# Performance work log

Measured on AMD Instinct MI355X. Metric: run time of the kernel, lower is better.

The kernel has to match this reference:

```python
import jax, jax.numpy as jnp
import numpy as np

# SuperposedExpert: K parallel TT-factorized FFN paths + holographic routing.
# d_model=1024 factorized as [32,32]; d_ff=4096 as [64,64]; tt_ranks=[1,16,1] (r0/r2 squeezed).
K, D_MODEL, D_FF, RANK = 4, 1024, 4096, 16
IN1, IN2 = 32, 32          # factorize_for_tt(d_model)
F1, F2 = 64, 64            # factorize_for_tt(d_ff)
TEMP = 1.0                 # routing_temperature


def setup_inputs() -> dict:
    key = jax.random.key(0)
    ks = jax.random.split(key, 8)
    s = 0.05
    tokens = jax.random.normal(ks[0], (2048, D_MODEL), dtype=jnp.float32)
    # TT cores for ffn1: d_model -> d_ff  (input_dims [32,32], output_dims [64,64])
    ffn1_core1 = jax.random.normal(ks[1], (K, IN1, F1, RANK), dtype=jnp.float32) * s
    ffn1_core2 = jax.random.normal(ks[2], (K, RANK, IN2, F2), dtype=jnp.float32) * s
    # TT cores for ffn2: d_ff -> d_model (input_dims [64,64], output_dims [32,32])
    ffn2_core1 = jax.random.normal(ks[3], (K, F1, IN1, RANK), dtype=jnp.float32) * s
    ffn2_core2 = jax.random.normal(ks[4], (K, RANK, F2, IN2), dtype=jnp.float32) * s
    # Holographic routing params (hd_dim == d_model -> identity HD projection)
    pb = jax.random.normal(ks[5], (K, D_MODEL), dtype=jnp.float32)
    path_bases = pb / jnp.linalg.norm(pb, axis=-1, keepdims=True)  # orthogonal-ish init
    path_weights = jax.random.normal(ks[6], (K, D_MODEL), dtype=jnp.float32) * s
    return {
        'tokens': tokens,
        'ffn1_core1': ffn1_core1, 'ffn1_core2': ffn1_core2,
        'ffn2_core1': ffn2_core1, 'ffn2_core2': ffn2_core2,
        'path_bases': path_bases, 'path_weights': path_weights,
    }


def reference(tokens, ffn1_core1, ffn1_core2, ffn2_core1, ffn2_core2,
              path_bases, path_weights):
    N = tokens.shape[0]
    # ---- K superposed TT-FFN paths ----
    x3 = tokens.reshape(N, IN1, IN2)  # [n, a, b]
    # TT matmul 1: y[x,y] = sum_{a,b,r} G1[a,x,r] G2[r,b,y] x[a,b]
    h = jnp.einsum('nab,kaxr,krby->knxy', x3, ffn1_core1, ffn1_core2)
    h = jax.nn.gelu(h.reshape(K, N, D_FF))  # quantum_activation stand-in
    h3 = h.reshape(K, N, F1, F2)
    y = jnp.einsum('knab,kaxr,krby->knxy', h3, ffn2_core1, ffn2_core2)
    y = y.reshape(K, N, D_MODEL)  # per-path outputs
    # ---- Holographic HD routing (hd_dim == d_model: identity projection) ----
    logits = jnp.einsum('nd,kd->nk', tokens, path_bases) / TEMP
    gates = jax.nn.softmax(logits, axis=-1)  # [n, k]
    # Collapse superposition: per-path elementwise HD modulation + gated sum
    out = jnp.einsum('knd,kd,nk->nd', y, 1.0 + path_weights, gates)
    return out
```

## Files before the change

### kernel.cpp

```cpp
#include <hip/hip_runtime.h>
#include <stdint.h>

#define GAS __attribute__((address_space(1)))
#define LAS __attribute__((address_space(3)))

typedef __attribute__((ext_vector_type(8))) short short8;
typedef __attribute__((ext_vector_type(16))) float f32x16;
typedef __attribute__((ext_vector_type(4))) float f32x4;

static constexpr int N_TOK = 2048;
static constexpr int DM    = 1024;
static constexpr int DF    = 4096;
static constexpr int KP    = 4;

__device__ inline unsigned short f2bf(float f) {
  union { float f; uint32_t u; } v; v.f = f;
  uint32_t u = v.u;
  u += 0x7FFFu + ((u >> 16) & 1u);
  return (unsigned short)(u >> 16);
}

__device__ inline uint32_t pk_bf(float lo, float hi) {
  union { float f; uint32_t u; } a, b; a.f = lo; b.f = hi;
  uint32_t ul = a.u + 0x7FFFu + ((a.u >> 16) & 1u);
  uint32_t uh = b.u + 0x7FFFu + ((b.u >> 16) & 1u);
  return (ul >> 16) | (uh & 0xFFFF0000u);
}

__device__ inline float gelu_gate(float v, float g) {
  float t0 = v * v;
  float u  = v * __builtin_fmaf(t0, -0.10294456f, -2.3022539f);
  float e  = __builtin_amdgcn_exp2f(u);
  float r  = __builtin_amdgcn_rcpf(1.0f + e);
  return v * g * r;
}

__device__ inline void gld16(const void* g, void* l) {
  __builtin_amdgcn_global_load_lds((const GAS void*)g, (LAS void*)l, 16, 0, 0);
}

__global__ __launch_bounds__(256) void setup_kernel(
    const float* __restrict__ tokens, const float* __restrict__ pb,
    const float* __restrict__ c11, const float* __restrict__ c12,
    const float* __restrict__ c21, const float* __restrict__ c22,
    float* __restrict__ gates, unsigned short* __restrict__ xb,
    unsigned short* __restrict__ w1t, unsigned short* __restrict__ w2t) {
  __shared__ __align__(16) float sh[17472];
  const int blk = blockIdx.x;
  const int t = threadIdx.x;
  if (blk < 1024) {
    const int k = blk >> 8, x = (blk >> 2) & 63, y0 = (blk & 3) * 16;
    float* s1  = sh;
    float* s2T = sh + 512;
    if (t < 128) {
      int a = t >> 2, rq = (t & 3) * 4;
      *(float4*)(s1 + a * 16 + rq) =
          *(const float4*)(c11 + (((size_t)(k * 32 + a)) * 64 + x) * 16 + rq);
    }
#pragma unroll
    for (int j = 0; j < 8; ++j) {
      int i = t + j * 256;
      int rb = i >> 2, yy0 = (i & 3) * 4;
      float4 v = *(const float4*)(c12 + (size_t)(k * 16) * 2048 + (size_t)rb * 64 + y0 + yy0);
      s2T[(yy0 + 0) * 524 + rb] = v.x;
      s2T[(yy0 + 1) * 524 + rb] = v.y;
      s2T[(yy0 + 2) * 524 + rb] = v.z;
      s2T[(yy0 + 3) * 524 + rb] = v.w;
    }
    __syncthreads();
    const int a = t >> 3, b0 = (t & 7) * 4;
    float4 s1q[4];
#pragma unroll
    for (int q = 0; q < 4; ++q) s1q[q] = *(const float4*)(s1 + a * 16 + q * 4);
    const float* a0s = (const float*)s1q;
    for (int y = 0; y < 16; ++y) {
      const float* s2y = s2T + y * 524;
      float4 acc = {0.f, 0.f, 0.f, 0.f};
#pragma unroll
      for (int r = 0; r < 16; ++r) {
        float cv = a0s[r];
        float4 bv = *(const float4*)(s2y + r * 32 + b0);
        acc.x = __builtin_fmaf(cv, bv.x, acc.x);
        acc.y = __builtin_fmaf(cv, bv.y, acc.y);
        acc.z = __builtin_fmaf(cv, bv.z, acc.z);
        acc.w = __builtin_fmaf(cv, bv.w, acc.w);
      }
      ushort4 o; o.x = f2bf(acc.x); o.y = f2bf(acc.y); o.z = f2bf(acc.z); o.w = f2bf(acc.w);
      *(ushort4*)(w1t + ((size_t)k * DF + x * 64 + y0 + y) * DM + t * 4) = o;
    }
  } else if (blk < 1280) {
    const int bb = blk - 1024;
    const int k = bb >> 6, x = (bb >> 1) & 31, y0 = (bb & 1) * 16;
    float* s1  = sh;
    float* s2T = sh + 1024;
    {
      int a = t >> 2, rq = (t & 3) * 4;
      *(float4*)(s1 + a * 16 + rq) =
          *(const float4*)(c21 + (((size_t)(k * 64 + a)) * 32 + x) * 16 + rq);
    }
#pragma unroll
    for (int j = 0; j < 16; ++j) {
      int i = t + j * 256;
      int rb = i >> 2, yy0 = (i & 3) * 4;
      float4 v = *(const float4*)(c22 + (size_t)(k * 16) * 2048 + (size_t)rb * 32 + y0 + yy0);
      s2T[(yy0 + 0) * 1028 + rb] = v.x;
      s2T[(yy0 + 1) * 1028 + rb] = v.y;
      s2T[(yy0 + 2) * 1028 + rb] = v.z;
      s2T[(yy0 + 3) * 1028 + rb] = v.w;
    }
    __syncthreads();
    const int b0 = (t & 15) * 4;
#pragma unroll
    for (int jj = 0; jj < 4; ++jj) {
      const int a = (t >> 4) + jj * 16;
      float4 s1q[4];
#pragma unroll
      for (int q = 0; q < 4; ++q) s1q[q] = *(const float4*)(s1 + a * 16 + q * 4);
      const float* a0s = (const float*)s1q;
      for (int y = 0; y < 16; ++y) {
        const float* s2y = s2T + y * 1028;
        float4 acc = {0.f, 0.f, 0.f, 0.f};
#pragma unroll
        for (int r = 0; r < 16; ++r) {
          float cv = a0s[r];
          float4 bv = *(const float4*)(s2y + r * 64 + b0);
          acc.x = __builtin_fmaf(cv, bv.x, acc.x);
          acc.y = __builtin_fmaf(cv, bv.y, acc.y);
          acc.z = __builtin_fmaf(cv, bv.z, acc.z);
          acc.w = __builtin_fmaf(cv, bv.w, acc.w);
        }
        ushort4 o; o.x = f2bf(acc.x); o.y = f2bf(acc.y); o.z = f2bf(acc.z); o.w = f2bf(acc.w);
        *(ushort4*)(w2t + ((size_t)k * DM + x * 32 + y0 + y) * DF + t * 4 + jj * 1024) = o;
      }
    }
  } else {
    const int wave = t >> 6, lane = t & 63;
    const int n = (blk - 1280) * 4 + wave;
    float s0 = 0.f, s1v = 0.f, s2v = 0.f, s3v = 0.f;
    const float4* tr = (const float4*)(tokens + (size_t)n * DM);
#pragma unroll
    for (int j = 0; j < 4; ++j) {
      int idx = j * 64 + lane;
      float4 tv = tr[idx];
      ushort4 b;
      b.x = f2bf(tv.x); b.y = f2bf(tv.y); b.z = f2bf(tv.z); b.w = f2bf(tv.w);
      *(ushort4*)(xb + (size_t)n * DM + idx * 4) = b;
      float4 q;
      q = ((const float4*)(pb + 0 * DM))[idx]; s0  += tv.x*q.x + tv.y*q.y + tv.z*q.z + tv.w*q.w;
      q = ((const float4*)(pb + 1 * DM))[idx]; s1v += tv.x*q.x + tv.y*q.y + tv.z*q.z + tv.w*q.w;
      q = ((const float4*)(pb + 2 * DM))[idx]; s2v += tv.x*q.x + tv.y*q.y + tv.z*q.z + tv.w*q.w;
      q = ((const float4*)(pb + 3 * DM))[idx]; s3v += tv.x*q.x + tv.y*q.y + tv.z*q.z + tv.w*q.w;
    }
#pragma unroll
    for (int off = 32; off > 0; off >>= 1) {
      s0  += __shfl_xor(s0, off);
      s1v += __shfl_xor(s1v, off);
      s2v += __shfl_xor(s2v, off);
      s3v += __shfl_xor(s3v, off);
    }
    if (lane == 0) {
      float m = fmaxf(fmaxf(s0, s1v), fmaxf(s2v, s3v));
      float e0 = __expf(s0 - m), e1 = __expf(s1v - m), e2 = __expf(s2v - m), e3 = __expf(s3v - m);
      float inv = 1.0f / (e0 + e1 + e2 + e3);
      float4 g; g.x = e0 * inv; g.y = e1 * inv; g.z = e2 * inv; g.w = e3 * inv;
      *(float4*)(gates + n * 4) = g;
    }
  }
}

#define PH_SYNC(V) do { \
    asm volatile("s_waitcnt vmcnt(" #V ")" ::: "memory"); \
    __builtin_amdgcn_s_barrier(); \
    __builtin_amdgcn_sched_barrier(0); \
  } while (0)

#define G1_TILE(KT, BO, WO, V0, V1, V2) do { \
    const int kn_ = ((KT) + 1) * 64; \
    const bool st_ = (KT) < 15; \
     \
    PH_SYNC(V0); \
    if (st_) { const unsigned short* s_ = Wg + (size_t)srow * DM + kn_ + lch * 8; \
      gld16(s_, smem + (WO) + t * 16); gld16(s_ + 64 * DM, smem + (WO) + 8192 + t * 16); } \
    _Pragma("unroll") for (int fi = 0; fi < 4; ++fi) \
      _Pragma("unroll") for (int s = 0; s < 2; ++s) \
        af[fi][s] = *(const short8*)(smem + (BO) + aRowB + fi * 2048 + (cxor16 ^ (s * 64) ^ (fi * 32))); \
    _Pragma("unroll") for (int ti = 0; ti < 2; ++ti) \
      _Pragma("unroll") for (int s = 0; s < 2; ++s) \
        bf0[ti][s] = *(const short8*)(smem + (BO) + xRowB + ti * 2048 + (cxor16 ^ (s * 64) ^ wnx64 ^ (ti * 32))); \
    __builtin_amdgcn_s_setprio(1); \
    _Pragma("unroll") for (int fi = 0; fi < 4; ++fi) \
      _Pragma("unroll") for (int ti = 0; ti < 2; ++ti) { \
        acc[0][0][fi][ti] = __builtin_amdgcn_mfma_f32_16x16x32_bf16(af[fi][0], bf0[ti][0], acc[0][0][fi][ti], 0, 0, 0); \
        acc[0][0][fi][ti] = __builtin_amdgcn_mfma_f32_16x16x32_bf16(af[fi][1], bf0[ti][1], acc[0][0][fi][ti], 0, 0, 0); } \
    __builtin_amdgcn_s_setprio(0); \
     \
    PH_SYNC(V1); \
    if (st_) { const unsigned short* s_ = Xg + (size_t)srow * DM + kn_ + lch * 8; \
      gld16(s_, smem + (WO) + 32768 + t * 16); gld16(s_ + 64 * DM, smem + (WO) + 32768 + 8192 + t * 16); } \
    _Pragma("unroll") for (int ti = 0; ti < 2; ++ti) \
      _Pragma("unroll") for (int s = 0; s < 2; ++s) \
        bf1[ti][s] = *(const short8*)(smem + (BO) + xRowB + 16384 + ti * 2048 + (cxor16 ^ (s * 64) ^ wnx64 ^ (ti * 32))); \
    __builtin_amdgcn_s_setprio(1); \
    _Pragma("unroll") for (int fi = 0; fi < 4; ++fi) \
      _Pragma("unroll") for (int ti = 0; ti < 2; ++ti) { \
        acc[0][1][fi][ti] = __builtin_amdgcn_mfma_f32_16x16x32_bf16(af[fi][0], bf1[ti][0], acc[0][1][fi][ti], 0, 0, 0); \
        acc[0][1][fi][ti] = __builtin_amdgcn_mfma_f32_16x16x32_bf16(af[fi][1], bf1[ti][1], acc[0][1][fi][ti], 0, 0, 0); } \
    __builtin_amdgcn_s_setprio(0); \
     \
    PH_SYNC(V2); \
    if (st_) { const unsigned short* s_ = Xg + (size_t)(128 + srow) * DM + kn_ + lch * 8; \
      gld16(s_, smem + (WO) + 32768 + 16384 + t * 16); gld16(s_ + 64 * DM, smem + (WO) + 32768 + 16384 + 8192 + t * 16); } \
    _Pragma("unroll") for (int fi = 0; fi < 4; ++fi) \
      _Pragma("unroll") for (int s = 0; s < 2; ++s) \
        af[fi][s] = *(const short8*)(smem + (BO) + aRowB + 16384 + fi * 2048 + (cxor16 ^ (s * 64) ^ (fi * 32))); \
    __builtin_amdgcn_s_setprio(1); \
    _Pragma("unroll") for (int fi = 0; fi < 4; ++fi) \
      _Pragma("unroll") for (int ti = 0; ti < 2; ++ti) { \
        acc[1][1][fi][ti] = __builtin_amdgcn_mfma_f32_16x16x32_bf16(af[fi][0], bf1[ti][0], acc[1][1][fi][ti], 0, 0, 0); \
        acc[1][1][fi][ti] = __builtin_amdgcn_mfma_f32_16x16x32_bf16(af[fi][1], bf1[ti][1], acc[1][1][fi][ti], 0, 0, 0); } \
    __builtin_amdgcn_s_setprio(0); \
     \
    if (st_) { const unsigned short* s_ = Wg + (size_t)(128 + srow) * DM + kn_ + lch * 8; \
      gld16(s_, smem + (WO) + 16384 + t * 16); gld16(s_ + 64 * DM, smem + (WO) + 16384 + 8192 + t * 16); } \
    __builtin_amdgcn_s_setprio(1); \
    _Pragma("unroll") for (int fi = 0; fi < 4; ++fi) \
      _Pragma("unroll") for (int ti = 0; ti < 2; ++ti) { \
        acc[1][0][fi][ti] = __builtin_amdgcn_mfma_f32_16x16x32_bf16(af[fi][0], bf0[ti][0], acc[1][0][fi][ti], 0, 0, 0); \
        acc[1][0][fi][ti] = __builtin_amdgcn_mfma_f32_16x16x32_bf16(af[fi][1], bf0[ti][1], acc[1][0][fi][ti], 0, 0, 0); } \
    __builtin_amdgcn_s_setprio(0); \
  } while (0)

__global__ __launch_bounds__(512, 1) void gemm1(
    const unsigned short* __restrict__ xb, const unsigned short* __restrict__ w1t,
    const float* __restrict__ gates, unsigned short* __restrict__ hg) {
  __shared__ __align__(16) char smem[131072];
  const int t = threadIdx.x, lane = t & 63, wv = t >> 6;
  const int wm = wv >> 2, wn = wv & 3;
  const int hw = blockIdx.x + (blockIdx.y << 3) + (blockIdx.z << 7);
  const int lg = (hw & 7) * 64 + (hw >> 3);
  const int m0 = (lg & 7) * 256;
  const int f0 = ((lg >> 3) & 15) * 256;
  const int kp = lg >> 7;
  const unsigned short* __restrict__ Wg = w1t + (size_t)kp * DF * DM + (size_t)f0 * DM;
  const unsigned short* __restrict__ Xg = xb + (size_t)m0 * DM;

  const int srow = t >> 3;
  const int lch  = (t & 7) ^ (srow & 7) ^ (srow >> 3);
  const int l15 = lane & 15, kg = lane >> 4;
  const int cxor16 = (kg ^ (lane & 7) ^ (l15 >> 3)) * 16;
  const int wnx64  = (wn & 1) * 64;
  const int aRowB  = (wm * 64 + l15) * 128;
  const int xRowB  = 32768 + (wn * 32 + l15) * 128;

  f32x4 acc[2][2][4][2] = {};
  short8 af[4][2], bf0[2][2], bf1[2][2];

  {
    const unsigned short* sw = Wg + (size_t)srow * DM + lch * 8;
    const unsigned short* sx = Xg + (size_t)srow * DM + lch * 8;
    gld16(sw,            smem + t * 16);
    gld16(sw + 64 * DM,  smem + 8192 + t * 16);
    gld16(sx,            smem + 32768 + t * 16);
    gld16(sx + 64 * DM,  smem + 32768 + 8192 + t * 16);
    gld16(sx + 128 * DM, smem + 32768 + 16384 + t * 16);
    gld16(sx + 192 * DM, smem + 32768 + 16384 + 8192 + t * 16);
    gld16(sw + 128 * DM, smem + 16384 + t * 16);
    gld16(sw + 192 * DM, smem + 16384 + 8192 + t * 16);
  }

#pragma unroll 1
  for (int kt = 0; kt < 14; kt += 2) {
    G1_TILE(kt,     0,     65536, 4, 4, 4);
    G1_TILE(kt + 1, 65536, 0,     4, 4, 4);
  }
  G1_TILE(14, 0,     65536, 4, 4, 4);
  G1_TILE(15, 65536, 0,     4, 2, 0);

  unsigned short* __restrict__ H = hg + (size_t)kp * N_TOK * DF;
#pragma unroll
  for (int cB = 0; cB < 2; ++cB)
#pragma unroll
    for (int ti = 0; ti < 2; ++ti) {
      const int tok = m0 + cB * 128 + wn * 32 + ti * 16 + l15;
      const float g = gates[tok * 4 + kp];
      unsigned short* hrow = H + (size_t)tok * DF + f0 + wm * 64 + kg * 4;
#pragma unroll
      for (int rA = 0; rA < 2; ++rA)
#pragma unroll
        for (int fi = 0; fi < 4; ++fi) {
          f32x4 v = acc[rA][cB][fi][ti];
          float r0 = gelu_gate(v.x, g);
          float r1 = gelu_gate(v.y, g);
          float r2 = gelu_gate(v.z, g);
          float r3 = gelu_gate(v.w, g);
          uint2 p; p.x = pk_bf(r0, r1); p.y = pk_bf(r2, r3);
          *(uint2*)(hrow + rA * 128 + fi * 16) = p;
        }
    }
}

#define G2_TILE(KT, BO, WO, V0, V1, V2) do { \
    const int kn_ = ((KT) + 1) * 64; \
    const bool st_ = (KT) < 63; \
     \
    PH_SYNC(V0); \
    if (st_) gld16(Wg + (size_t)srow * DF + kn_ + lch * 8, smem + (WO) + t * 16); \
    _Pragma("unroll") for (int fi = 0; fi < 2; ++fi) \
      _Pragma("unroll") for (int s = 0; s < 2; ++s) \
        af[fi][s] = *(const short8*)(smem + (BO) + awRowB + fi * 2048 + (cxor16 ^ awx ^ (fi * 32) ^ (s * 64))); \
    _Pragma("unroll") for (int ti = 0; ti < 2; ++ti) \
      _Pragma("unroll") for (int s = 0; s < 2; ++s) \
        bf0[ti][s] = *(const short8*)(smem + (BO) + xRowB + ti * 2048 + (cxor16 ^ wnx64 ^ (ti * 32) ^ (s * 64))); \
    __builtin_amdgcn_s_setprio(1); \
    _Pragma("unroll") for (int fi = 0; fi < 2; ++fi) \
      _Pragma("unroll") for (int ti = 0; ti < 2; ++ti) { \
        acc[0][0][fi][ti] = __builtin_amdgcn_mfma_f32_16x16x32_bf16(af[fi][0], bf0[ti][0], acc[0][0][fi][ti], 0, 0, 0); \
        acc[0][0][fi][ti] = __builtin_amdgcn_mfma_f32_16x16x32_bf16(af[fi][1], bf0[ti][1], acc[0][0][fi][ti], 0, 0, 0); } \
    __builtin_amdgcn_s_setprio(0); \
     \
    PH_SYNC(V1); \
    if (st_) { const unsigned short* s_ = Xg + (size_t)srow * DF + kn_ + lch * 8; \
      gld16(s_, smem + (WO) + 16384 + t * 16); gld16(s_ + 64 * DF, smem + (WO) + 16384 + 8192 + t * 16); } \
    _Pragma("unroll") for (int ti = 0; ti < 2; ++ti) \
      _Pragma("unroll") for (int s = 0; s < 2; ++s) \
        bf1[ti][s] = *(const short8*)(smem + (BO) + xRowB + 16384 + ti * 2048 + (cxor16 ^ wnx64 ^ (ti * 32) ^ (s * 64))); \
    __builtin_amdgcn_s_setprio(1); \
    _Pragma("unroll") for (int fi = 0; fi < 2; ++fi) \
      _Pragma("unroll") for (int ti = 0; ti < 2; ++ti) { \
        acc[0][1][fi][ti] = __builtin_amdgcn_mfma_f32_16x16x32_bf16(af[fi][0], bf1[ti][0], acc[0][1][fi][ti], 0, 0, 0); \
        acc[0][1][fi][ti] = __builtin_amdgcn_mfma_f32_16x16x32_bf16(af[fi][1], bf1[ti][1], acc[0][1][fi][ti], 0, 0, 0); } \
    __builtin_amdgcn_s_setprio(0); \
     \
    PH_SYNC(V2); \
    if (st_) { const unsigned short* s_ = Xg + (size_t)(128 + srow) * DF + kn_ + lch * 8; \
      gld16(s_, smem + (WO) + 32768 + t * 16); gld16(s_ + 64 * DF, smem + (WO) + 32768 + 8192 + t * 16); } \
    _Pragma("unroll") for (int fi = 0; fi < 2; ++fi) \
      _Pragma("unroll") for (int s = 0; s < 2; ++s) \
        af[fi][s] = *(const short8*)(smem + (BO) + awRowB + 8192 + fi * 2048 + (cxor16 ^ awx ^ (fi * 32) ^ (s * 64))); \
    __builtin_amdgcn_s_setprio(1); \
    _Pragma("unroll") for (int fi = 0; fi < 2; ++fi) \
      _Pragma("unroll") for (int ti = 0; ti < 2; ++ti) { \
        acc[1][1][fi][ti] = __builtin_amdgcn_mfma_f32_16x16x32_bf16(af[fi][0], bf1[ti][0], acc[1][1][fi][ti], 0, 0, 0); \
        acc[1][1][fi][ti] = __builtin_amdgcn_mfma_f32_16x16x32_bf16(af[fi][1], bf1[ti][1], acc[1][1][fi][ti], 0, 0, 0); } \
    __builtin_amdgcn_s_setprio(0); \
     \
    if (st_) gld16(Wg + (size_t)(64 + srow) * DF + kn_ + lch * 8, smem + (WO) + 8192 + t * 16); \
    __builtin_amdgcn_s_setprio(1); \
    _Pragma("unroll") for (int fi = 0; fi < 2; ++fi) \
      _Pragma("unroll") for (int ti = 0; ti < 2; ++ti) { \
        acc[1][0][fi][ti] = __builtin_amdgcn_mfma_f32_16x16x32_bf16(af[fi][0], bf0[ti][0], acc[1][0][fi][ti], 0, 0, 0); \
        acc[1][0][fi][ti] = __builtin_amdgcn_mfma_f32_16x16x32_bf16(af[fi][1], bf0[ti][1], acc[1][0][fi][ti], 0, 0, 0); } \
    __builtin_amdgcn_s_setprio(0); \
  } while (0)

__global__ __launch_bounds__(512, 1) void gemm2(
    const unsigned short* __restrict__ hg, const unsigned short* __restrict__ w2t,
    const float* __restrict__ pw, float* __restrict__ part) {
  __shared__ __align__(16) char smem[98304];
  const int t = threadIdx.x, lane = t & 63, wv = t >> 6;
  const int wm = wv >> 2, wn = wv & 3;
  const int hw = blockIdx.x + (blockIdx.y << 3) + (blockIdx.z << 6);
  const int lg = (hw & 7) * 32 + (hw >> 3);
  const int m0 = (lg & 7) * 256;
  const int n0 = ((lg >> 3) & 7) * 128;
  const int kp = lg >> 6;
  const unsigned short* __restrict__ Wg = w2t + (size_t)kp * DM * DF + (size_t)n0 * DF;
  const unsigned short* __restrict__ Xg = hg + (size_t)kp * N_TOK * DF + (size_t)m0 * DF;

  const int srow = t >> 3;
  const int lch  = (t & 7) ^ (srow & 7) ^ (srow >> 3);
  const int l15 = lane & 15, kg = lane >> 4;
  const int cxor16 = (kg ^ (lane & 7) ^ (l15 >> 3)) * 16;
  const int wnx64  = (wn & 1) * 64;
  const int awx    = wm * 64;
  const int awRowB = (wm * 32 + l15) * 128;
  const int xRowB  = 16384 + (wn * 32 + l15) * 128;

  f32x4 acc[2][2][2][2] = {};
  short8 af[2][2], bf0[2][2], bf1[2][2];

  {
    const unsigned short* sw = Wg + (size_t)srow * DF + lch * 8;
    const unsigned short* sx = Xg + (size_t)srow * DF + lch * 8;
    gld16(sw,            smem + t * 16);
    gld16(sx,            smem + 16384 + t * 16);
    gld16(sx + 64 * DF,  smem + 16384 + 8192 + t * 16);
    gld16(sx + 128 * DF, smem + 32768 + t * 16);
    gld16(sx + 192 * DF, smem + 32768 + 8192 + t * 16);
    gld16(sw + 64 * DF,  smem + 8192 + t * 16);
  }

#pragma unroll 1
  for (int kt = 0; kt < 62; kt += 2) {
    G2_TILE(kt,     0,     49152, 3, 2, 3);
    G2_TILE(kt + 1, 49152, 0,     3, 2, 3);
  }
  G2_TILE(62, 0,     49152, 3, 2, 3);
  G2_TILE(63, 49152, 0,     3, 1, 0);

  float* __restrict__ P = part + (size_t)kp * N_TOK * DM;
  float4 pwv[2][2];
#pragma unroll
  for (int rA = 0; rA < 2; ++rA)
#pragma unroll
    for (int fi = 0; fi < 2; ++fi) {
      float4 w = *(const float4*)(pw + kp * DM + n0 + rA * 64 + wm * 32 + fi * 16 + kg * 4);
      pwv[rA][fi].x = 1.0f + w.x; pwv[rA][fi].y = 1.0f + w.y;
      pwv[rA][fi].z = 1.0f + w.z; pwv[rA][fi].w = 1.0f + w.w;
    }
#pragma unroll
  for (int cB = 0; cB < 2; ++cB)
#pragma unroll
    for (int ti = 0; ti < 2; ++ti) {
      const int tok = m0 + cB * 128 + wn * 32 + ti * 16 + l15;
      float* prow = P + (size_t)tok * DM + n0 + wm * 32 + kg * 4;
#pragma unroll
      for (int rA = 0; rA < 2; ++rA)
#pragma unroll
        for (int fi = 0; fi < 2; ++fi) {
          f32x4 v = acc[rA][cB][fi][ti];
          float4 o;
          o.x = pwv[rA][fi].x * v.x;
          o.y = pwv[rA][fi].y * v.y;
          o.z = pwv[rA][fi].z * v.z;
          o.w = pwv[rA][fi].w * v.w;
          *(float4*)(prow + rA * 64 + fi * 16) = o;
        }
    }
}

__global__ __launch_bounds__(256) void reduce_k(
    const float* __restrict__ part, float* __restrict__ out) {
  const size_t i = ((size_t)blockIdx.x * 256 + threadIdx.x) * 4;
  const size_t S = (size_t)N_TOK * DM;
  float4 a = *(const float4*)(part + i);
  float4 b = *(const float4*)(part + S + i);
  float4 c = *(const float4*)(part + 2 * S + i);
  float4 d = *(const float4*)(part + 3 * S + i);
  float4 r;
  r.x = a.x + b.x + c.x + d.x;
  r.y = a.y + b.y + c.y + d.y;
  r.z = a.z + b.z + c.z + d.z;
  r.w = a.w + b.w + c.w + d.w;
  *(float4*)(out + i) = r;
}

extern "C" void kernel_launch(void* const* d_in, const int* in_sizes, int n_in,
                              void* d_out, int out_size, void* d_ws, size_t ws_size,
                              hipStream_t stream) {
  const float* tokens = (const float*)d_in[0];
  const float* f1c1   = (const float*)d_in[1];
  const float* f1c2   = (const float*)d_in[2];
  const float* f2c1   = (const float*)d_in[3];
  const float* f2c2   = (const float*)d_in[4];
  const float* pb     = (const float*)d_in[5];
  const float* pw     = (const float*)d_in[6];
  float* out = (float*)d_out;

  char* ws = (char*)d_ws;
  unsigned short* xb  = (unsigned short*)(ws);
  unsigned short* w1t = (unsigned short*)(ws + (4ull  << 20));
  float*          part = (float*)(ws + (4ull << 20));
  unsigned short* w2t = (unsigned short*)(ws + (36ull << 20));
  unsigned short* hg  = (unsigned short*)(ws + (68ull << 20));
  float*          gates = (float*)(ws + (132ull << 20));

  hipLaunchKernelGGL(setup_kernel, dim3(1792), dim3(256), 0, stream,
                     tokens, pb, f1c1, f1c2, f2c1, f2c2, gates, xb, w1t, w2t);
  hipLaunchKernelGGL(gemm1, dim3(8, 16, KP), dim3(512), 0, stream, xb, w1t, gates, hg);
  hipLaunchKernelGGL(gemm2, dim3(8, 8, KP), dim3(512), 0, stream, hg, w2t, pw, part);
  hipLaunchKernelGGL(reduce_k, dim3(2048), dim3(256), 0, stream, part, out);
}
```

Measured before the change: 243.9 us.

## Prefetch next tile's A/B fragments into registers across phases in both GEMMs

Restructures the per-tile phase schedule of both GEMM kernels so that the first A and B fragments of the next K-tile are loaded from LDS during the last phase of the current tile. Separate lo/hi A-fragment registers and ping-ponged B0 buffers are added, and the vmcnt wait points are reordered. The goal is to hide LDS read latency behind MFMA work and cut stalls at the start of each tile. In exchange, register pressure goes up at one block per CU, and the reworked wait counts must still cover every outstanding global-to-LDS load.

```diff
diff --git a/kernel.cpp b/kernel.cpp
--- a/kernel.cpp
+++ b/kernel.cpp
@@ -168,67 +168,68 @@
   }
 }
 
-#define PH_SYNC(V) do { \
-    asm volatile("s_waitcnt vmcnt(" #V ")" ::: "memory"); \
-    __builtin_amdgcn_s_barrier(); \
-    __builtin_amdgcn_sched_barrier(0); \
-  } while (0)
-
-#define G1_TILE(KT, BO, WO, V0, V1, V2) do { \
-    const int kn_ = ((KT) + 1) * 64; \
-    const bool st_ = (KT) < 15; \
-     \
-    PH_SYNC(V0); \
-    if (st_) { const unsigned short* s_ = Wg + (size_t)srow * DM + kn_ + lch * 8; \
-      gld16(s_, smem + (WO) + t * 16); gld16(s_ + 64 * DM, smem + (WO) + 8192 + t * 16); } \
+#define VMC(N) asm volatile("s_waitcnt vmcnt(" #N ")" ::: "memory")
+#define BARS do { __builtin_amdgcn_s_barrier(); __builtin_amdgcn_sched_barrier(0); } while (0)
+
+#define G1T(KT, BO, WO, B0C, B0N, V0S, V1S, PREF3) do { \
+  const int kn_ = ((KT) + 1) * 64; \
+  const bool st_ = (KT) < 15; \
+   \
+  VMC(V0S); BARS; \
+  _Pragma("unroll") for (int ti = 0; ti < 2; ++ti) \
+    _Pragma("unroll") for (int s = 0; s < 2; ++s) \
+      bf1[ti][s] = *(const short8*)(smem + (BO) + xRowB + 16384 + ti * 2048 + (cxor16 ^ (s * 64) ^ wnx64 ^ (ti * 32))); \
+  if (st_) { const unsigned short* s_ = Wg + (size_t)srow * DM + kn_ + lch * 8; \
+    gld16(s_, smem + (WO) + t * 16); gld16(s_ + 64 * DM, smem + (WO) + 8192 + t * 16); } \
+  __builtin_amdgcn_s_setprio(1); \
+  _Pragma("unroll") for (int fi = 0; fi < 4; ++fi) \
+    _Pragma("unroll") for (int ti = 0; ti < 2; ++ti) { \
+      acc[0][0][fi][ti] = __builtin_amdgcn_mfma_f32_16x16x32_bf16(af_lo[fi][0], B0C[ti][0], acc[0][0][fi][ti], 0, 0, 0); \
+      acc[0][0][fi][ti] = __builtin_amdgcn_mfma_f32_16x16x32_bf16(af_lo[fi][1], B0C[ti][1], acc[0][0][fi][ti], 0, 0, 0); } \
+  __builtin_amdgcn_s_setprio(0); \
+   \
+  VMC(V1S); BARS; \
+  _Pragma("unroll") for (int fi = 0; fi < 4; ++fi) \
+    _Pragma("unroll") for (int s = 0; s < 2; ++s) \
+      af_hi[fi][s] = *(const short8*)(smem + (BO) + aRowB + 16384 + fi * 2048 + (cxor16 ^ (s * 64) ^ (fi * 32))); \
+  if (st_) { const unsigned short* s_ = Xg + (size_t)srow * DM + kn_ + lch * 8; \
+    gld16(s_, smem + (WO) + 32768 + t * 16); gld16(s_ + 64 * DM, smem + (WO) + 32768 + 8192 + t * 16); } \
+  __builtin_amdgcn_s_setprio(1); \
+  _Pragma("unroll") for (int fi = 0; fi < 4; ++fi) \
+    _Pragma("unroll") for (int ti = 0; ti < 2; ++ti) { \
+      acc[0][1][fi][ti] = __builtin_amdgcn_mfma_f32_16x16x32_bf16(af_lo[fi][0], bf1[ti][0], acc[0][1][fi][ti], 0, 0, 0); \
+      acc[0][1][fi][ti] = __builtin_amdgcn_mfma_f32_16x16x32_bf16(af_lo[fi][1], bf1[ti][1], acc[0][1][fi][ti], 0, 0, 0); } \
+  __builtin_amdgcn_s_setprio(0); \
+   \
+  BARS; \
+  if (st_) { const unsigned short* s_ = Xg + (size_t)(128 + srow) * DM + kn_ + lch * 8; \
+    gld16(s_, smem + (WO) + 32768 + 16384 + t * 16); gld16(s_ + 64 * DM, smem + (WO) + 32768 + 16384 + 8192 + t * 16); } \
+  __builtin_amdgcn_s_setprio(1); \
+  _Pragma("unroll") for (int fi = 0; fi < 4; ++fi) \
+    _Pragma("unroll") for (int ti = 0; ti < 2; ++ti) { \
+      acc[1][1][fi][ti] = __builtin_amdgcn_mfma_f32_16x16x32_bf16(af_hi[fi][0], bf1[ti][0], acc[1][1][fi][ti], 0, 0, 0); \
+      acc[1][1][fi][ti] = __builtin_amdgcn_mfma_f32_16x16x32_bf16(af_hi[fi][1], bf1[ti][1], acc[1][1][fi][ti], 0, 0, 0); } \
+  __builtin_amdgcn_s_setprio(0); \
+   \
+  if (PREF3) { VMC(2); } \
+  BARS; \
+  if (PREF3) { \
     _Pragma("unroll") for (int fi = 0; fi < 4; ++fi) \
       _Pragma("unroll") for (int s = 0; s < 2; ++s) \
-        af[fi][s] = *(const short8*)(smem + (BO) + aRowB + fi * 2048 + (cxor16 ^ (s * 64) ^ (fi * 32))); \
+        af_lo[fi][s] = *(const short8*)(smem + (WO) + aRowB + fi * 2048 + (cxor16 ^ (s * 64) ^ (fi * 32))); \
     _Pragma("unroll") for (int ti = 0; ti < 2; ++ti) \
       _Pragma("unroll") for (int s = 0; s < 2; ++s) \
-        bf0[ti][s] = *(const short8*)(smem + (BO) + xRowB + ti * 2048 + (cxor16 ^ (s * 64) ^ wnx64 ^ (ti * 32))); \
-    __builtin_amdgcn_s_setprio(1); \
-    _Pragma("unroll") for (int fi = 0; fi < 4; ++fi) \
-      _Pragma("unroll") for (int ti = 0; ti < 2; ++ti) { \
-        acc[0][0][fi][ti] = __builtin_amdgcn_mfma_f32_16x16x32_bf16(af[fi][0], bf0[ti][0], acc[0][0][fi][ti], 0, 0, 0); \
-        acc[0][0][fi][ti] = __builtin_amdgcn_mfma_f32_16x16x32_bf16(af[fi][1], bf0[ti][1], acc[0][0][fi][ti], 0, 0, 0); } \
-    __builtin_amdgcn_s_setprio(0); \
-     \
-    PH_SYNC(V1); \
-    if (st_) { const unsigned short* s_ = Xg + (size_t)srow * DM + kn_ + lch * 8; \
-      gld16(s_, smem + (WO) + 32768 + t * 16); gld16(s_ + 64 * DM, smem + (WO) + 32768 + 8192 + t * 16); } \
-    _Pragma("unroll") for (int ti = 0; ti < 2; ++ti) \
-      _Pragma("unroll") for (int s = 0; s < 2; ++s) \
-        bf1[ti][s] = *(const short8*)(smem + (BO) + xRowB + 16384 + ti * 2048 + (cxor16 ^ (s * 64) ^ wnx64 ^ (ti * 32))); \
-    __builtin_amdgcn_s_setprio(1); \
-    _Pragma("unroll") for (int fi = 0; fi < 4; ++fi) \
-      _Pragma("unroll") for (int ti = 0; ti < 2; ++ti) { \
-        acc[0][1][fi][ti] = __builtin_amdgcn_mfma_f32_16x16x32_bf16(af[fi][0], bf1[ti][0], acc[0][1][fi][ti], 0, 0, 0); \
-        acc[0][1][fi][ti] = __builtin_amdgcn_mfma_f32_16x16x32_bf16(af[fi][1], bf1[ti][1], acc[0][1][fi][ti], 0, 0, 0); } \
-    __builtin_amdgcn_s_setprio(0); \
-     \
-    PH_SYNC(V2); \
-    if (st_) { const unsigned short* s_ = Xg + (size_t)(128 + srow) * DM + kn_ + lch * 8; \
-      gld16(s_, smem + (WO) + 32768 + 16384 + t * 16); gld16(s_ + 64 * DM, smem + (WO) + 32768 + 16384 + 8192 + t * 16); } \
-    _Pragma("unroll") for (int fi = 0; fi < 4; ++fi) \
-      _Pragma("unroll") for (int s = 0; s < 2; ++s) \
-        af[fi][s] = *(const short8*)(smem + (BO) + aRowB + 16384 + fi * 2048 + (cxor16 ^ (s * 64) ^ (fi * 32))); \
-    __builtin_amdgcn_s_setprio(1); \
-    _Pragma("unroll") for (int fi = 0; fi < 4; ++fi) \
-      _Pragma("unroll") for (int ti = 0; ti < 2; ++ti) { \
-        acc[1][1][fi][ti] = __builtin_amdgcn_mfma_f32_16x16x32_bf16(af[fi][0], bf1[ti][0], acc[1][1][fi][ti], 0, 0, 0); \
-        acc[1][1][fi][ti] = __builtin_amdgcn_mfma_f32_16x16x32_bf16(af[fi][1], bf1[ti][1], acc[1][1][fi][ti], 0, 0, 0); } \
-    __builtin_amdgcn_s_setprio(0); \
-     \
-    if (st_) { const unsigned short* s_ = Wg + (size_t)(128 + srow) * DM + kn_ + lch * 8; \
-      gld16(s_, smem + (WO) + 16384 + t * 16); gld16(s_ + 64 * DM, smem + (WO) + 16384 + 8192 + t * 16); } \
-    __builtin_amdgcn_s_setprio(1); \
-    _Pragma("unroll") for (int fi = 0; fi < 4; ++fi) \
-      _Pragma("unroll") for (int ti = 0; ti < 2; ++ti) { \
-        acc[1][0][fi][ti] = __builtin_amdgcn_mfma_f32_16x16x32_bf16(af[fi][0], bf0[ti][0], acc[1][0][fi][ti], 0, 0, 0); \
-        acc[1][0][fi][ti] = __builtin_amdgcn_mfma_f32_16x16x32_bf16(af[fi][1], bf0[ti][1], acc[1][0][fi][ti], 0, 0, 0); } \
-    __builtin_amdgcn_s_setprio(0); \
-  } while (0)
+        B0N[ti][s] = *(const short8*)(smem + (WO) + xRowB + ti * 2048 + (cxor16 ^ (s * 64) ^ wnx64 ^ (ti * 32))); \
+  } \
+  if (st_) { const unsigned short* s_ = Wg + (size_t)(128 + srow) * DM + kn_ + lch * 8; \
+    gld16(s_, smem + (WO) + 16384 + t * 16); gld16(s_ + 64 * DM, smem + (WO) + 16384 + 8192 + t * 16); } \
+  __builtin_amdgcn_s_setprio(1); \
+  _Pragma("unroll") for (int fi = 0; fi < 4; ++fi) \
+    _Pragma("unroll") for (int ti = 0; ti < 2; ++ti) { \
+      acc[1][0][fi][ti] = __builtin_amdgcn_mfma_f32_16x16x32_bf16(af_hi[fi][0], B0C[ti][0], acc[1][0][fi][ti], 0, 0, 0); \
+      acc[1][0][fi][ti] = __builtin_amdgcn_mfma_f32_16x16x32_bf16(af_hi[fi][1], B0C[ti][1], acc[1][0][fi][ti], 0, 0, 0); } \
+  __builtin_amdgcn_s_setprio(0); \
+} while (0)
 
 __global__ __launch_bounds__(512, 1) void gemm1(
     const unsigned short* __restrict__ xb, const unsigned short* __restrict__ w1t,
@@ -253,7 +254,7 @@
   const int xRowB  = 32768 + (wn * 32 + l15) * 128;
 
   f32x4 acc[2][2][4][2] = {};
-  short8 af[4][2], bf0[2][2], bf1[2][2];
+  short8 af_lo[4][2], af_hi[4][2], bf0p[2][2], bf0q[2][2], bf1[2][2];
 
   {
     const unsigned short* sw = Wg + (size_t)srow * DM + lch * 8;
@@ -267,14 +268,25 @@
     gld16(sw + 128 * DM, smem + 16384 + t * 16);
     gld16(sw + 192 * DM, smem + 16384 + 8192 + t * 16);
   }
+  VMC(4); BARS;
+#pragma unroll
+  for (int fi = 0; fi < 4; ++fi)
+#pragma unroll
+    for (int s = 0; s < 2; ++s)
+      af_lo[fi][s] = *(const short8*)(smem + aRowB + fi * 2048 + (cxor16 ^ (s * 64) ^ (fi * 32)));
+#pragma unroll
+  for (int ti = 0; ti < 2; ++ti)
+#pragma unroll
+    for (int s = 0; s < 2; ++s)
+      bf0p[ti][s] = *(const short8*)(smem + xRowB + ti * 2048 + (cxor16 ^ (s * 64) ^ wnx64 ^ (ti * 32)));
 
 #pragma unroll 1
   for (int kt = 0; kt < 14; kt += 2) {
-    G1_TILE(kt,     0,     65536, 4, 4, 4);
-    G1_TILE(kt + 1, 65536, 0,     4, 4, 4);
+    G1T(kt,     0,     65536, bf0p, bf0q, 2, 2, 1);
+    G1T(kt + 1, 65536, 0,     bf0q, bf0p, 2, 2, 1);
   }
-  G1_TILE(14, 0,     65536, 4, 4, 4);
-  G1_TILE(15, 65536, 0,     4, 2, 0);
+  G1T(14, 0,     65536, bf0p, bf0q, 2, 2, 1);
+  G1T(15, 65536, 0,     bf0q, bf0p, 2, 0, 0);
 
   unsigned short* __restrict__ H = hg + (size_t)kp * N_TOK * DF;
 #pragma unroll
@@ -299,59 +311,63 @@
     }
 }
 
-#define G2_TILE(KT, BO, WO, V0, V1, V2) do { \
-    const int kn_ = ((KT) + 1) * 64; \
-    const bool st_ = (KT) < 63; \
-     \
-    PH_SYNC(V0); \
-    if (st_) gld16(Wg + (size_t)srow * DF + kn_ + lch * 8, smem + (WO) + t * 16); \
+#define G2T(KT, BO, WO, B0C, B0N, V0S, V1S, PREF3) do { \
+  const int kn_ = ((KT) + 1) * 64; \
+  const bool st_ = (KT) < 63; \
+   \
+  VMC(V0S); BARS; \
+  _Pragma("unroll") for (int ti = 0; ti < 2; ++ti) \
+    _Pragma("unroll") for (int s = 0; s < 2; ++s) \
+      bf1[ti][s] = *(const short8*)(smem + (BO) + xRowB + 16384 + ti * 2048 + (cxor16 ^ wnx64 ^ (ti * 32) ^ (s * 64))); \
+  if (st_) gld16(Wg + (size_t)srow * DF + kn_ + lch * 8, smem + (WO) + t * 16); \
+  __builtin_amdgcn_s_setprio(1); \
+  _Pragma("unroll") for (int fi = 0; fi < 2; ++fi) \
+    _Pragma("unroll") for (int ti = 0; ti < 2; ++ti) { \
+      acc[0][0][fi][ti] = __builtin_amdgcn_mfma_f32_16x16x32_bf16(af_lo[fi][0], B0C[ti][0], acc[0][0][fi][ti], 0, 0, 0); \
+      acc[0][0][fi][ti] = __builtin_amdgcn_mfma_f32_16x16x32_bf16(af_lo[fi][1], B0C[ti][1], acc[0][0][fi][ti], 0, 0, 0); } \
+  __builtin_amdgcn_s_setprio(0); \
+   \
+  VMC(V1S); BARS; \
+  _Pragma("unroll") for (int fi = 0; fi < 2; ++fi) \
+    _Pragma("unroll") for (int s = 0; s < 2; ++s) \
+      af_hi[fi][s] = *(const short8*)(smem + (BO) + awRowB + 8192 + fi * 2048 + (cxor16 ^ awx ^ (fi * 32) ^ (s * 64))); \
+  if (st_) { const unsigned short* s_ = Xg + (size_t)srow * DF + kn_ + lch * 8; \
+    gld16(s_, smem + (WO) + 16384 + t * 16); gld16(s_ + 64 * DF, smem + (WO) + 16384 + 8192 + t * 16); } \
+  __builtin_amdgcn_s_setprio(1); \
+  _Pragma("unroll") for (int fi = 0; fi < 2; ++fi) \
+    _Pragma("unroll") for (int ti = 0; ti < 2; ++ti) { \
+      acc[0][1][fi][ti] = __builtin_amdgcn_mfma_f32_16x16x32_bf16(af_lo[fi][0], bf1[ti][0], acc[0][1][fi][ti], 0, 0, 0); \
+      acc[0][1][fi][ti] = __builtin_amdgcn_mfma_f32_16x16x32_bf16(af_lo[fi][1], bf1[ti][1], acc[0][1][fi][ti], 0, 0, 0); } \
+  __builtin_amdgcn_s_setprio(0); \
+   \
+  BARS; \
+  if (st_) { const unsigned short* s_ = Xg + (size_t)(128 + srow) * DF + kn_ + lch * 8; \
+    gld16(s_, smem + (WO) + 32768 + t * 16); gld16(s_ + 64 * DF, smem + (WO) + 32768 + 8192 + t * 16); } \
+  __builtin_amdgcn_s_setprio(1); \
+  _Pragma("unroll") for (int fi = 0; fi < 2; ++fi) \
+    _Pragma("unroll") for (int ti = 0; ti < 2; ++ti) { \
+      acc[1][1][fi][ti] = __builtin_amdgcn_mfma_f32_16x16x32_bf16(af_hi[fi][0], bf1[ti][0], acc[1][1][fi][ti], 0, 0, 0); \
+      acc[1][1][fi][ti] = __builtin_amdgcn_mfma_f32_16x16x32_bf16(af_hi[fi][1], bf1[ti][1], acc[1][1][fi][ti], 0, 0, 0); } \
+  __builtin_amdgcn_s_setprio(0); \
+   \
+  if (PREF3) { VMC(2); } \
+  BARS; \
+  if (PREF3) { \
     _Pragma("unroll") for (int fi = 0; fi < 2; ++fi) \
       _Pragma("unroll") for (int s = 0; s < 2; ++s) \
-        af[fi][s] = *(const short8*)(smem + (BO) + awRowB + fi * 2048 + (cxor16 ^ awx ^ (fi * 32) ^ (s * 64))); \
+        af_lo[fi][s] = *(const short8*)(smem + (WO) + awRowB + fi * 2048 + (cxor16 ^ awx ^ (fi * 32) ^ (s * 64))); \
     _Pragma("unroll") for (int ti = 0; ti < 2; ++ti) \
       _Pragma("unroll") for (int s = 0; s < 2; ++s) \
-        bf0[ti][s] = *(const short8*)(smem + (BO) + xRowB + ti * 2048 + (cxor16 ^ wnx64 ^ (ti * 32) ^ (s * 64))); \
-    __builtin_amdgcn_s_setprio(1); \
-    _Pragma("unroll") for (int fi = 0; fi < 2; ++fi) \
-      _Pragma("unroll") for (int ti = 0; ti < 2; ++ti) { \
-        acc[0][0][fi][ti] = __builtin_amdgcn_mfma_f32_16x16x32_bf16(af[fi][0], bf0[ti][0], acc[0][0][fi][ti], 0, 0, 0); \
-        acc[0][0][fi][ti] = __builtin_amdgcn_mfma_f32_16x16x32_bf16(af[fi][1], bf0[ti][1], acc[0][0][fi][ti], 0, 0, 0); } \
-    __builtin_amdgcn_s_setprio(0); \
-     \
-    PH_SYNC(V1); \
-    if (st_) { const unsigned short* s_ = Xg + (size_t)srow * DF + kn_ + lch * 8; \
-      gld16(s_, smem + (WO) + 16384 + t * 16); gld16(s_ + 64 * DF, smem + (WO) + 16384 + 8192 + t * 16); } \
-    _Pragma("unroll") for (int ti = 0; ti < 2; ++ti) \
-      _Pragma("unroll") for (int s = 0; s < 2; ++s) \
-        bf1[ti][s] = *(const short8*)(smem + (BO) + xRowB + 16384 + ti * 2048 + (cxor16 ^ wnx64 ^ (ti * 32) ^ (s * 64))); \
-    __builtin_amdgcn_s_setprio(1); \
-    _Pragma("unroll") for (int fi = 0; fi < 2; ++fi) \
-      _Pragma("unroll") for (int ti = 0; ti < 2; ++ti) { \
-        acc[0][1][fi][ti] = __builtin_amdgcn_mfma_f32_16x16x32_bf16(af[fi][0], bf1[ti][0], acc[0][1][fi][ti], 0, 0, 0); \
-        acc[0][1][fi][ti] = __builtin_amdgcn_mfma_f32_16x16x32_bf16(af[fi][1], bf1[ti][1], acc[0][1][fi][ti], 0, 0, 0); } \
-    __builtin_amdgcn_s_setprio(0); \
-     \
-    PH_SYNC(V2); \
-    if (st_) { const unsigned short* s_ = Xg + (size_t)(128 + srow) * DF + kn_ + lch * 8; \
-      gld16(s_, smem + (WO) + 32768 + t * 16); gld16(s_ + 64 * DF, smem + (WO) + 32768 + 8192 + t * 16); } \
-    _Pragma("unroll") for (int fi = 0; fi < 2; ++fi) \
-      _Pragma("unroll") for (int s = 0; s < 2; ++s) \
-        af[fi][s] = *(const short8*)(smem + (BO) + awRowB + 8192 + fi * 2048 + (cxor16 ^ awx ^ (fi * 32) ^ (s * 64))); \
-    __builtin_amdgcn_s_setprio(1); \
-    _Pragma("unroll") for (int fi = 0; fi < 2; ++fi) \
-      _Pragma("unroll") for (int ti = 0; ti < 2; ++ti) { \
-        acc[1][1][fi][ti] = __builtin_amdgcn_mfma_f32_16x16x32_bf16(af[fi][0], bf1[ti][0], acc[1][1][fi][ti], 0, 0, 0); \
-        acc[1][1][fi][ti] = __builtin_amdgcn_mfma_f32_16x16x32_bf16(af[fi][1], bf1[ti][1], acc[1][1][fi][ti], 0, 0, 0); } \
-    __builtin_amdgcn_s_setprio(0); \
-     \
-    if (st_) gld16(Wg + (size_t)(64 + srow) * DF + kn_ + lch * 8, smem + (WO) + 8192 + t * 16); \
-    __builtin_amdgcn_s_setprio(1); \
-    _Pragma("unroll") for (int fi = 0; fi < 2; ++fi) \
-      _Pragma("unroll") for (int ti = 0; ti < 2; ++ti) { \
-        acc[1][0][fi][ti] = __builtin_amdgcn_mfma_f32_16x16x32_bf16(af[fi][0], bf0[ti][0], acc[1][0][fi][ti], 0, 0, 0); \
-        acc[1][0][fi][ti] = __builtin_amdgcn_mfma_f32_16x16x32_bf16(af[fi][1], bf0[ti][1], acc[1][0][fi][ti], 0, 0, 0); } \
-    __builtin_amdgcn_s_setprio(0); \
-  } while (0)
+        B0N[ti][s] = *(const short8*)(smem + (WO) + xRowB + ti * 2048 + (cxor16 ^ wnx64 ^ (ti * 32) ^ (s * 64))); \
+  } \
+  if (st_) gld16(Wg + (size_t)(64 + srow) * DF + kn_ + lch * 8, smem + (WO) + 8192 + t * 16); \
+  __builtin_amdgcn_s_setprio(1); \
+  _Pragma("unroll") for (int fi = 0; fi < 2; ++fi) \
+    _Pragma("unroll") for (int ti = 0; ti < 2; ++ti) { \
+      acc[1][0][fi][ti] = __builtin_amdgcn_mfma_f32_16x16x32_bf16(af_hi[fi][0], B0C[ti][0], acc[1][0][fi][ti], 0, 0, 0); \
+      acc[1][0][fi][ti] = __builtin_amdgcn_mfma_f32_16x16x32_bf16(af_hi[fi][1], B0C[ti][1], acc[1][0][fi][ti], 0, 0, 0); } \
+  __builtin_amdgcn_s_setprio(0); \
+} while (0)
 
 __global__ __launch_bounds__(512, 1) void gemm2(
     const unsigned short* __restrict__ hg, const unsigned short* __restrict__ w2t,
@@ -377,7 +393,7 @@
   const int xRowB  = 16384 + (wn * 32 + l15) * 128;
 
   f32x4 acc[2][2][2][2] = {};
-  short8 af[2][2], bf0[2][2], bf1[2][2];
+  short8 af_lo[2][2], af_hi[2][2], bf0p[2][2], bf0q[2][2], bf1[2][2];
 
   {
     const unsigned short* sw = Wg + (size_t)srow * DF + lch * 8;
@@ -389,14 +405,25 @@
     gld16(sx + 192 * DF, smem + 32768 + 8192 + t * 16);
     gld16(sw + 64 * DF,  smem + 8192 + t * 16);
   }
+  VMC(3); BARS;
+#pragma unroll
+  for (int fi = 0; fi < 2; ++fi)
+#pragma unroll
+    for (int s = 0; s < 2; ++s)
+      af_lo[fi][s] = *(const short8*)(smem + awRowB + fi * 2048 + (cxor16 ^ awx ^ (fi * 32) ^ (s * 64)));
+#pragma unroll
+  for (int ti = 0; ti < 2; ++ti)
+#pragma unroll
+    for (int s = 0; s < 2; ++s)
+      bf0p[ti][s] = *(const short8*)(smem + xRowB + ti * 2048 + (cxor16 ^ wnx64 ^ (ti * 32) ^ (s * 64)));
 
 #pragma unroll 1
   for (int kt = 0; kt < 62; kt += 2) {
-    G2_TILE(kt,     0,     49152, 3, 2, 3);
-    G2_TILE(kt + 1, 49152, 0,     3, 2, 3);
+    G2T(kt,     0,     49152, bf0p, bf0q, 1, 1, 1);
+    G2T(kt + 1, 49152, 0,     bf0q, bf0p, 1, 1, 1);
   }
-  G2_TILE(62, 0,     49152, 3, 2, 3);
-  G2_TILE(63, 49152, 0,     3, 1, 0);
+  G2T(62, 0,     49152, bf0p, bf0q, 1, 1, 1);
+  G2T(63, 49152, 0,     bf0q, bf0p, 1, 0, 0);
 
   float* __restrict__ P = part + (size_t)kp * N_TOK * DM;
   float4 pwv[2][2];
```

Result: slower. 257.6 us (+5.6%).
